# Optimization experiments

Measured on AMD Instinct MI355X. Metric: run time of the kernel, lower is better.

Reference implementation:

```python
import jax, jax.numpy as jnp
import numpy as np

N_HEAD = 16
D_MODEL = 1024
D_K = 64
D_V = 64
LN_EPS = 1e-6


def setup_inputs() -> dict:
    key = jax.random.key(0)
    ks = jax.random.split(key, 10)
    B, S = 2, 2048
    scale = 0.02
    return {
        "q": jax.random.normal(ks[0], (B, S, D_MODEL), jnp.float32),
        "k": jax.random.normal(ks[1], (B, S, D_MODEL), jnp.float32),
        "v": jax.random.normal(ks[2], (B, S, D_MODEL), jnp.float32),
        "Wq": jax.random.normal(ks[3], (D_MODEL, N_HEAD * D_K), jnp.float32) * scale,
        "Wk": jax.random.normal(ks[4], (D_MODEL, N_HEAD * D_K), jnp.float32) * scale,
        "Wv": jax.random.normal(ks[5], (D_MODEL, N_HEAD * D_V), jnp.float32) * scale,
        "Wfc": jax.random.normal(ks[6], (N_HEAD * D_V, D_MODEL), jnp.float32) * scale,
        "bfc": jnp.zeros((D_MODEL,), jnp.float32),
        "gamma": jnp.ones((D_MODEL,), jnp.float32),
        "beta": jnp.zeros((D_MODEL,), jnp.float32),
    }


def reference(q, k, v, Wq, Wk, Wv, Wfc, bfc, gamma, beta):
    B, S, _ = q.shape
    residual = q
    # QKV projections, split into heads: [B, S, H, Dh]
    qh = (q @ Wq).reshape(B, S, N_HEAD, D_K)
    kh = (k @ Wk).reshape(B, S, N_HEAD, D_K)
    vh = (v @ Wv).reshape(B, S, N_HEAD, D_V)
    # scaled dot-product attention (explicit score matrix, as in source)
    temperature = jnp.asarray(D_K, qh.dtype) ** 0.5
    attn = jnp.einsum("bqhd,bkhd->bhqk", qh, kh) / temperature
    attn = jax.nn.softmax(attn, axis=-1)
    out = jnp.einsum("bhqk,bkhd->bqhd", attn, vh).reshape(B, S, N_HEAD * D_V)
    # output projection (dropout is identity in eval mode)
    out = out @ Wfc + bfc
    # residual + layernorm (eps=1e-6)
    x = out + residual
    mu = jnp.mean(x, axis=-1, keepdims=True)
    var = jnp.mean(jnp.square(x - mu), axis=-1, keepdims=True)
    return (x - mu) / jnp.sqrt(var + LN_EPS) * gamma + beta
```

## Files before the change

kernel.cpp:

```cpp
#include <hip/hip_runtime.h>

typedef float f32x4 __attribute__((ext_vector_type(4)));
typedef short short8 __attribute__((ext_vector_type(8)));
typedef short short4v __attribute__((ext_vector_type(4)));
typedef unsigned short ushort_t;

#define D_MODEL 1024
#define N_HEAD 16
#define SEQ 2048
#define BATCH 2
#define M_TOK 4096
#define HD 1024
#define QSCALE_L2E 0.1803368801111f

__device__ __forceinline__ ushort_t f2bf(float f) {
    union { float f; unsigned int u; } x; x.f = f;
    unsigned int r = x.u + 0x7fffu + ((x.u >> 16) & 1u);
    return (ushort_t)(r >> 16);
}
__device__ __forceinline__ ushort_t f2bf_fast(float f) {
    union { float f; unsigned int u; } x; x.f = f;
    return (ushort_t)((x.u + 0x8000u) >> 16);
}

__device__ __forceinline__ void async_copy16(const ushort_t* gptr, ushort_t* lptr) {
    __builtin_amdgcn_global_load_lds(
        (const __attribute__((address_space(1))) unsigned int*)gptr,
        (__attribute__((address_space(3))) unsigned int*)lptr, 16, 0, 0);
}

__global__ __launch_bounds__(256) void transpose_cast4(const float* __restrict__ w0,
                                                       const float* __restrict__ w1,
                                                       const float* __restrict__ w2,
                                                       const float* __restrict__ w3,
                                                       ushort_t* __restrict__ o0,
                                                       ushort_t* __restrict__ o1,
                                                       ushort_t* __restrict__ o2,
                                                       ushort_t* __restrict__ o3) {
    const int R = D_MODEL, C = D_MODEL;
    int z = blockIdx.z;
    const float* in = (z == 0) ? w0 : (z == 1) ? w1 : (z == 2) ? w2 : w3;
    ushort_t* out = (z == 0) ? o0 : (z == 1) ? o1 : (z == 2) ? o2 : o3;
    __shared__ ushort_t t[32][33];
    int bc = blockIdx.x * 32, br = blockIdx.y * 32;
    for (int i = threadIdx.y; i < 32; i += 8)
        t[i][threadIdx.x] = f2bf(in[(size_t)(br + i) * C + bc + threadIdx.x]);
    __syncthreads();
    for (int i = threadIdx.y; i < 32; i += 8)
        out[(size_t)(bc + i) * R + br + threadIdx.x] = t[threadIdx.x][i];
}

__global__ __launch_bounds__(256) void cast_bf16_3(const float* __restrict__ q,
                                                   const float* __restrict__ k,
                                                   const float* __restrict__ v,
                                                   ushort_t* __restrict__ qo,
                                                   ushort_t* __restrict__ ko,
                                                   ushort_t* __restrict__ vo) {
    int z = blockIdx.z;
    const float* s = (z == 0) ? q : (z == 1) ? k : v;
    ushort_t* d = (z == 0) ? qo : (z == 1) ? ko : vo;
    size_t i = ((size_t)blockIdx.x * 256 + threadIdx.x) * 8;
    float4 a = *(const float4*)(s + i);
    float4 b = *(const float4*)(s + i + 4);
    ushort_t tmp[8] = {f2bf(a.x), f2bf(a.y), f2bf(a.z), f2bf(a.w),
                       f2bf(b.x), f2bf(b.y), f2bf(b.z), f2bf(b.w)};
    *(short8*)(d + i) = *(short8*)tmp;
}

__global__ __launch_bounds__(256) void gemm_qkv(const ushort_t* __restrict__ qb,
                                                const ushort_t* __restrict__ kb,
                                                const ushort_t* __restrict__ vb,
                                                const ushort_t* __restrict__ wq,
                                                const ushort_t* __restrict__ wk,
                                                const ushort_t* __restrict__ wv,
                                                ushort_t* __restrict__ Qo,
                                                ushort_t* __restrict__ Ko,
                                                ushort_t* __restrict__ VtO) {
    __shared__ ushort_t As[128 * 32];
    __shared__ ushort_t Bs[128 * 32];
    const int z = blockIdx.z;
    const ushort_t* A = (z == 0) ? qb : (z == 1) ? kb : vb;
    const ushort_t* Bt = (z == 0) ? wq : (z == 1) ? wk : wv;
    const int tid = threadIdx.x;
    const int wave = tid >> 6, lane = tid & 63;
    const int quad = lane >> 4, l16 = lane & 15;
    const int m0 = blockIdx.y * 128, n0 = blockIdx.x * 128;
    const int wm = (wave >> 1) * 64, wn = (wave & 1) * 64;
    const int K = D_MODEL, N = D_MODEL;

    f32x4 acc[4][4];
    for (int i = 0; i < 4; ++i)
        for (int j = 0; j < 4; ++j) acc[i][j] = (f32x4){0.f, 0.f, 0.f, 0.f};

    for (int kk = 0; kk < K; kk += 32) {
        __syncthreads();
        #pragma unroll
        for (int c = 0; c < 2; ++c) {
            int flat = ((wave * 2 + c) * 64 + lane) * 8;
            int r = flat >> 5, col = flat & 31;
            async_copy16(Bt + (size_t)(n0 + r) * K + kk + col, &Bs[(wave * 2 + c) * 512]);
            async_copy16(A + (size_t)(m0 + r) * K + kk + col, &As[(wave * 2 + c) * 512]);
        }
        __syncthreads();
        short8 af[4], bfr[4];
        #pragma unroll
        for (int i = 0; i < 4; ++i)
            af[i] = *(const short8*)&As[(wm + i * 16 + l16) * 32 + quad * 8];
        #pragma unroll
        for (int j = 0; j < 4; ++j)
            bfr[j] = *(const short8*)&Bs[(wn + j * 16 + l16) * 32 + quad * 8];
        #pragma unroll
        for (int i = 0; i < 4; ++i)
            #pragma unroll
            for (int j = 0; j < 4; ++j)
                acc[i][j] = __builtin_amdgcn_mfma_f32_16x16x32_bf16(af[i], bfr[j], acc[i][j], 0, 0, 0);
    }
    if (z == 2) {
        #pragma unroll
        for (int i = 0; i < 4; ++i)
            #pragma unroll
            for (int j = 0; j < 4; ++j) {
                int n = n0 + wn + j * 16 + l16;
                int m = m0 + wm + i * 16 + quad * 4;
                ushort_t tmp[4];
                #pragma unroll
                for (int r = 0; r < 4; ++r) tmp[r] = f2bf(acc[i][j][r]);
                *(short4v*)&VtO[(size_t)n * M_TOK + m] = *(short4v*)tmp;
            }
    } else {
        ushort_t* C = (z == 0) ? Qo : Ko;
        const float scale = (z == 0) ? QSCALE_L2E : 1.0f;
        #pragma unroll
        for (int i = 0; i < 4; ++i)
            #pragma unroll
            for (int j = 0; j < 4; ++j) {
                int n = n0 + wn + j * 16 + l16;
                #pragma unroll
                for (int r = 0; r < 4; ++r) {
                    int m = m0 + wm + i * 16 + quad * 4 + r;
                    C[(size_t)m * N + n] = f2bf(acc[i][j][r] * scale);
                }
            }
    }
}

__global__ __launch_bounds__(256) void gemm_fc(const ushort_t* __restrict__ A,
                                               const ushort_t* __restrict__ Bt,
                                               float* __restrict__ Cf,
                                               const float* __restrict__ bias,
                                               const float* __restrict__ resid) {
    __shared__ ushort_t As[128 * 32];
    __shared__ ushort_t Bs[128 * 32];
    const int tid = threadIdx.x;
    const int wave = tid >> 6, lane = tid & 63;
    const int quad = lane >> 4, l16 = lane & 15;
    const int m0 = blockIdx.y * 128, n0 = blockIdx.x * 128;
    const int wm = (wave >> 1) * 64, wn = (wave & 1) * 64;
    const int K = D_MODEL, N = D_MODEL;

    f32x4 acc[4][4];
    for (int i = 0; i < 4; ++i)
        for (int j = 0; j < 4; ++j) acc[i][j] = (f32x4){0.f, 0.f, 0.f, 0.f};

    for (int kk = 0; kk < K; kk += 32) {
        __syncthreads();
        #pragma unroll
        for (int c = 0; c < 2; ++c) {
            int flat = ((wave * 2 + c) * 64 + lane) * 8;
            int r = flat >> 5, col = flat & 31;
            async_copy16(Bt + (size_t)(n0 + r) * K + kk + col, &Bs[(wave * 2 + c) * 512]);
            async_copy16(A + (size_t)(m0 + r) * K + kk + col, &As[(wave * 2 + c) * 512]);
        }
        __syncthreads();
        short8 af[4], bfr[4];
        #pragma unroll
        for (int i = 0; i < 4; ++i)
            af[i] = *(const short8*)&As[(wm + i * 16 + l16) * 32 + quad * 8];
        #pragma unroll
        for (int j = 0; j < 4; ++j)
            bfr[j] = *(const short8*)&Bs[(wn + j * 16 + l16) * 32 + quad * 8];
        #pragma unroll
        for (int i = 0; i < 4; ++i)
            #pragma unroll
            for (int j = 0; j < 4; ++j)
                acc[i][j] = __builtin_amdgcn_mfma_f32_16x16x32_bf16(af[i], bfr[j], acc[i][j], 0, 0, 0);
    }
    #pragma unroll
    for (int i = 0; i < 4; ++i)
        #pragma unroll
        for (int j = 0; j < 4; ++j) {
            int n = n0 + wn + j * 16 + l16;
            #pragma unroll
            for (int r = 0; r < 4; ++r) {
                int m = m0 + wm + i * 16 + quad * 4 + r;
                Cf[(size_t)m * N + n] = acc[i][j][r] + bias[n] + resid[(size_t)m * N + n];
            }
        }
}

__global__ __launch_bounds__(256, 3) void attn64(const ushort_t* __restrict__ Qh,
                                                 const ushort_t* __restrict__ Kh,
                                                 const ushort_t* __restrict__ Vt,
                                                 ushort_t* __restrict__ O) {
    __shared__ ushort_t KVs[16768];
    __shared__ float lsb[4 * 64];
    const int tid = threadIdx.x;
    const int wave = tid >> 6, lane = tid & 63;
    const int quad = lane >> 4, l16 = lane & 15;
    const int b = blockIdx.z, h = blockIdx.y, qt = blockIdx.x;
    const size_t base = (size_t)b * SEQ * HD + h * 64;
    const ushort_t* Qb = Qh + base + (size_t)(qt * 64) * HD;
    const ushort_t* Kb = Kh + base;
    const ushort_t* Vb = Vt + (size_t)(h * 64) * M_TOK + (size_t)b * SEQ;

    ushort_t* Kw = KVs + wave * 2048;
    ushort_t* Vw = KVs + 8192 + wave * 2048;

    short8 qf[4][2];
    #pragma unroll
    for (int nt = 0; nt < 4; ++nt)
        #pragma unroll
        for (int s = 0; s < 2; ++s)
            qf[nt][s] = *(const short8*)(Qb + (size_t)(nt * 16 + l16) * HD + s * 32 + quad * 8);

    f32x4 oacc[4][4];
    #pragma unroll
    for (int nt = 0; nt < 4; ++nt)
        #pragma unroll
        for (int dt = 0; dt < 4; ++dt) oacc[nt][dt] = (f32x4){0.f, 0.f, 0.f, 0.f};
    float lsum[4] = {0.f, 0.f, 0.f, 0.f};

    const ushort_t* Kg = Kb + (size_t)(wave * 16 + (lane >> 2)) * HD + (lane & 3) * 8;
    const ushort_t* Vg = Vb + (size_t)(lane >> 1) * M_TOK + wave * 16 + (lane & 1) * 8;
    ushort_t* KL = Kw + lane * 8;
    ushort_t* VL = Vw + lane * 8;

    #pragma unroll
    for (int c = 0; c < 2; ++c) {
        async_copy16(Kg + c * 32, KL + c * 512);
        async_copy16(Vg + (size_t)c * 32 * M_TOK, VL + c * 512);
    }

    #pragma unroll 2
    for (int kt = 0; kt < SEQ / 64; ++kt) {
        const int buf = kt & 1;
        __builtin_amdgcn_s_waitcnt(0x0F70);
        if (kt < SEQ / 64 - 1) {
            #pragma unroll
            for (int c = 0; c < 2; ++c) {
                async_copy16(Kg + (size_t)(kt + 1) * 64 * HD + c * 32,
                             KL + (buf ^ 1) * 1024 + c * 512);
                async_copy16(Vg + (size_t)c * 32 * M_TOK + (kt + 1) * 64,
                             VL + (buf ^ 1) * 1024 + c * 512);
            }
        }
        short8 kf[2];
        #pragma unroll
        for (int s = 0; s < 2; ++s)
            kf[s] = *(const short8*)&Kw[buf * 1024 + s * 512 + l16 * 32 + quad * 8];
        short4v vf[4];
        #pragma unroll
        for (int dt = 0; dt < 4; ++dt)
            vf[dt] = *(const short4v*)&Vw[buf * 1024 + (dt * 16 + l16) * 16 + quad * 4];

        f32x4 sacc[4];
        #pragma unroll
        for (int nt = 0; nt < 4; ++nt) sacc[nt] = (f32x4){0.f, 0.f, 0.f, 0.f};
        #pragma unroll
        for (int s = 0; s < 2; ++s)
            #pragma unroll
            for (int nt = 0; nt < 4; ++nt)
                sacc[nt] = __builtin_amdgcn_mfma_f32_16x16x32_bf16(kf[s], qf[nt][s], sacc[nt], 0, 0, 0);

        short4v pf[4];
        #pragma unroll
        for (int nt = 0; nt < 4; ++nt) {
            ushort_t tmp[4];
            #pragma unroll
            for (int i = 0; i < 4; ++i) {
                float pv = exp2f(sacc[nt][i]);
                lsum[nt] += pv;
                tmp[i] = f2bf_fast(pv);
            }
            pf[nt] = *(short4v*)tmp;
        }
        #pragma unroll
        for (int nt = 0; nt < 4; ++nt)
            #pragma unroll
            for (int dt = 0; dt < 4; ++dt)
                oacc[nt][dt] = __builtin_amdgcn_mfma_f32_16x16x16bf16_1k(pf[nt], vf[dt], oacc[nt][dt], 0, 0, 0);
    }

    #pragma unroll
    for (int nt = 0; nt < 4; ++nt) {
        lsum[nt] += __shfl_xor(lsum[nt], 16, 64);
        lsum[nt] += __shfl_xor(lsum[nt], 32, 64);
    }
    if (quad == 0) {
        #pragma unroll
        for (int nt = 0; nt < 4; ++nt) lsb[wave * 64 + nt * 16 + l16] = lsum[nt];
    }
    __syncthreads();

    float* R0 = (float*)KVs;
    float* R1 = R0 + 64 * 65;
    {
        float* R = (wave & 1) ? R1 : R0;
        if (wave < 2) {
            #pragma unroll
            for (int nt = 0; nt < 4; ++nt)
                #pragma unroll
                for (int dt = 0; dt < 4; ++dt)
                    #pragma unroll
                    for (int i = 0; i < 4; ++i)
                        R[(nt * 16 + quad * 4 + i) * 65 + dt * 16 + l16] = oacc[nt][dt][i];
        }
        __syncthreads();
        if (wave >= 2) {
            #pragma unroll
            for (int nt = 0; nt < 4; ++nt)
                #pragma unroll
                for (int dt = 0; dt < 4; ++dt)
                    #pragma unroll
                    for (int i = 0; i < 4; ++i)
                        R[(nt * 16 + quad * 4 + i) * 65 + dt * 16 + l16] += oacc[nt][dt][i];
        }
        __syncthreads();
    }
    float inv[4];
    #pragma unroll
    for (int i = 0; i < 4; ++i) {
        int qrow = wave * 16 + quad * 4 + i;
        float t = lsb[qrow] + lsb[64 + qrow] + lsb[128 + qrow] + lsb[192 + qrow];
        inv[i] = 1.f / t;
    }
    ushort_t* Ob = O + base + (size_t)(qt * 64) * HD;
    #pragma unroll
    for (int i = 0; i < 4; ++i) {
        int qrow = wave * 16 + quad * 4 + i;
        #pragma unroll
        for (int dt = 0; dt < 4; ++dt) {
            int d = dt * 16 + l16;
            float val = R0[qrow * 65 + d] + R1[qrow * 65 + d];
            Ob[(size_t)qrow * HD + d] = f2bf(val * inv[i]);
        }
    }
}

__global__ __launch_bounds__(256) void ln_kernel(float* __restrict__ x,
                                                 const float* __restrict__ gamma,
                                                 const float* __restrict__ beta) {
    const int D = D_MODEL;
    float* xr = x + (size_t)blockIdx.x * D;
    const int tid = threadIdx.x;
    float4 v = *(const float4*)(xr + tid * 4);
    float s = v.x + v.y + v.z + v.w;
    float s2 = v.x * v.x + v.y * v.y + v.z * v.z + v.w * v.w;
    #pragma unroll
    for (int off = 1; off < 64; off <<= 1) {
        s += __shfl_xor(s, off, 64);
        s2 += __shfl_xor(s2, off, 64);
    }
    __shared__ float ws1[4], ws2[4];
    int wave = tid >> 6, lane = tid & 63;
    if (lane == 0) { ws1[wave] = s; ws2[wave] = s2; }
    __syncthreads();
    s = ws1[0] + ws1[1] + ws1[2] + ws1[3];
    s2 = ws2[0] + ws2[1] + ws2[2] + ws2[3];
    float mean = s * (1.f / D);
    float var = s2 * (1.f / D) - mean * mean;
    float rstd = rsqrtf(var + 1e-6f);
    float4 g = *(const float4*)(gamma + tid * 4);
    float4 bt = *(const float4*)(beta + tid * 4);
    float4 o;
    o.x = (v.x - mean) * rstd * g.x + bt.x;
    o.y = (v.y - mean) * rstd * g.y + bt.y;
    o.z = (v.z - mean) * rstd * g.z + bt.z;
    o.w = (v.w - mean) * rstd * g.w + bt.w;
    *(float4*)(xr + tid * 4) = o;
}

extern "C" void kernel_launch(void* const* d_in, const int* in_sizes, int n_in,
                              void* d_out, int out_size, void* d_ws, size_t ws_size,
                              hipStream_t stream) {
    const float* q = (const float*)d_in[0];
    const float* k = (const float*)d_in[1];
    const float* v = (const float*)d_in[2];
    const float* Wq = (const float*)d_in[3];
    const float* Wk = (const float*)d_in[4];
    const float* Wv = (const float*)d_in[5];
    const float* Wfc = (const float*)d_in[6];
    const float* bfc = (const float*)d_in[7];
    const float* gamma = (const float*)d_in[8];
    const float* beta = (const float*)d_in[9];
    float* out = (float*)d_out;

    char* ws = (char*)d_ws;
    const size_t MB = 1u << 20;
    ushort_t* WqT  = (ushort_t*)(ws + 0 * MB);
    ushort_t* WkT  = (ushort_t*)(ws + 2 * MB);
    ushort_t* WvT  = (ushort_t*)(ws + 4 * MB);
    ushort_t* WfcT = (ushort_t*)(ws + 6 * MB);
    ushort_t* qb   = (ushort_t*)(ws + 8 * MB);
    ushort_t* kb   = (ushort_t*)(ws + 16 * MB);
    ushort_t* vb   = (ushort_t*)(ws + 24 * MB);
    ushort_t* Qh   = (ushort_t*)(ws + 32 * MB);
    ushort_t* Kh   = (ushort_t*)(ws + 40 * MB);
    ushort_t* Vt   = (ushort_t*)(ws + 48 * MB);
    ushort_t* Oh   = (ushort_t*)(ws + 8 * MB);

    const int M = M_TOK, D = D_MODEL;
    transpose_cast4<<<dim3(D / 32, D / 32, 4), dim3(32, 8), 0, stream>>>(
        Wq, Wk, Wv, Wfc, WqT, WkT, WvT, WfcT);

    cast_bf16_3<<<dim3(M * D / (256 * 8), 1, 3), 256, 0, stream>>>(q, k, v, qb, kb, vb);

    gemm_qkv<<<dim3(D / 128, M / 128, 3), 256, 0, stream>>>(qb, kb, vb, WqT, WkT, WvT, Qh, Kh, Vt);

    attn64<<<dim3(SEQ / 64, N_HEAD, BATCH), 256, 0, stream>>>(Qh, Kh, Vt, Oh);

    gemm_fc<<<dim3(D / 128, M / 128), 256, 0, stream>>>(Oh, WfcT, out, bfc, q);

    ln_kernel<<<M, 256, 0, stream>>>(out, gamma, beta);
}
```

Before: 271.9 us.

## Load K to registers, triple-buffer swizzled V in attention, shrink FC tile

In the attention kernel, K fragments now go straight from global memory into registers with one-tile-ahead prefetch. V is triple-buffered in LDS and read with a rotated (swizzled) quad layout that matches a swizzled Vt write in the QKV GEMM epilogue, which is meant to reduce LDS bank conflicts. exp2f becomes the hardware builtin. Separately, the FC GEMM tile goes from 128x128 to 128x64, doubling the block count for better occupancy on many CUs.

Result: faster. 258.0 us (-5.1%).

```diff
diff --git a/kernel.cpp b/kernel.cpp
--- a/kernel.cpp
+++ b/kernel.cpp
@@ -11,6 +11,7 @@
 #define BATCH 2
 #define M_TOK 4096
 #define HD 1024
+#define NT 32
 #define QSCALE_L2E 0.1803368801111f
 
 __device__ __forceinline__ ushort_t f2bf(float f) {
@@ -121,11 +122,12 @@
             #pragma unroll
             for (int j = 0; j < 4; ++j) {
                 int n = n0 + wn + j * 16 + l16;
-                int m = m0 + wm + i * 16 + quad * 4;
+                int mBase = m0 + wm + i * 16;
+                int quadR = (quad + (n >> 2)) & 3;
                 ushort_t tmp[4];
                 #pragma unroll
                 for (int r = 0; r < 4; ++r) tmp[r] = f2bf(acc[i][j][r]);
-                *(short4v*)&VtO[(size_t)n * M_TOK + m] = *(short4v*)tmp;
+                *(short4v*)&VtO[(size_t)n * M_TOK + mBase + quadR * 4] = *(short4v*)tmp;
             }
     } else {
         ushort_t* C = (z == 0) ? Qo : Ko;
@@ -150,49 +152,53 @@
                                                const float* __restrict__ bias,
                                                const float* __restrict__ resid) {
     __shared__ ushort_t As[128 * 32];
-    __shared__ ushort_t Bs[128 * 32];
+    __shared__ ushort_t Bs[64 * 32];
     const int tid = threadIdx.x;
     const int wave = tid >> 6, lane = tid & 63;
     const int quad = lane >> 4, l16 = lane & 15;
-    const int m0 = blockIdx.y * 128, n0 = blockIdx.x * 128;
-    const int wm = (wave >> 1) * 64, wn = (wave & 1) * 64;
+    const int m0 = blockIdx.y * 128, n0 = blockIdx.x * 64;
     const int K = D_MODEL, N = D_MODEL;
 
-    f32x4 acc[4][4];
-    for (int i = 0; i < 4; ++i)
+    f32x4 acc[2][4];
+    for (int i = 0; i < 2; ++i)
         for (int j = 0; j < 4; ++j) acc[i][j] = (f32x4){0.f, 0.f, 0.f, 0.f};
 
     for (int kk = 0; kk < K; kk += 32) {
         __syncthreads();
         #pragma unroll
         for (int c = 0; c < 2; ++c) {
-            int flat = ((wave * 2 + c) * 64 + lane) * 8;
+            int g = wave * 2 + c;
+            int flat = (g * 64 + lane) * 8;
             int r = flat >> 5, col = flat & 31;
-            async_copy16(Bt + (size_t)(n0 + r) * K + kk + col, &Bs[(wave * 2 + c) * 512]);
-            async_copy16(A + (size_t)(m0 + r) * K + kk + col, &As[(wave * 2 + c) * 512]);
-        }
-        __syncthreads();
-        short8 af[4], bfr[4];
-        #pragma unroll
-        for (int i = 0; i < 4; ++i)
-            af[i] = *(const short8*)&As[(wm + i * 16 + l16) * 32 + quad * 8];
+            async_copy16(A + (size_t)(m0 + r) * K + kk + col, &As[g * 512]);
+        }
+        {
+            int flat = (wave * 64 + lane) * 8;
+            int r = flat >> 5, col = flat & 31;
+            async_copy16(Bt + (size_t)(n0 + r) * K + kk + col, &Bs[wave * 512]);
+        }
+        __syncthreads();
+        short8 af[2], bfr[4];
+        #pragma unroll
+        for (int i = 0; i < 2; ++i)
+            af[i] = *(const short8*)&As[(wave * 32 + i * 16 + l16) * 32 + quad * 8];
         #pragma unroll
         for (int j = 0; j < 4; ++j)
-            bfr[j] = *(const short8*)&Bs[(wn + j * 16 + l16) * 32 + quad * 8];
-        #pragma unroll
-        for (int i = 0; i < 4; ++i)
+            bfr[j] = *(const short8*)&Bs[(j * 16 + l16) * 32 + quad * 8];
+        #pragma unroll
+        for (int i = 0; i < 2; ++i)
             #pragma unroll
             for (int j = 0; j < 4; ++j)
                 acc[i][j] = __builtin_amdgcn_mfma_f32_16x16x32_bf16(af[i], bfr[j], acc[i][j], 0, 0, 0);
     }
     #pragma unroll
-    for (int i = 0; i < 4; ++i)
+    for (int i = 0; i < 2; ++i)
         #pragma unroll
         for (int j = 0; j < 4; ++j) {
-            int n = n0 + wn + j * 16 + l16;
+            int n = n0 + j * 16 + l16;
             #pragma unroll
             for (int r = 0; r < 4; ++r) {
-                int m = m0 + wm + i * 16 + quad * 4 + r;
+                int m = m0 + wave * 32 + i * 16 + quad * 4 + r;
                 Cf[(size_t)m * N + n] = acc[i][j][r] + bias[n] + resid[(size_t)m * N + n];
             }
         }
@@ -202,8 +208,7 @@
                                                  const ushort_t* __restrict__ Kh,
                                                  const ushort_t* __restrict__ Vt,
                                                  ushort_t* __restrict__ O) {
-    __shared__ ushort_t KVs[16768];
-    __shared__ float lsb[4 * 64];
+    __shared__ __align__(16) char smem[34304];
     const int tid = threadIdx.x;
     const int wave = tid >> 6, lane = tid & 63;
     const int quad = lane >> 4, l16 = lane & 15;
@@ -213,8 +218,8 @@
     const ushort_t* Kb = Kh + base;
     const ushort_t* Vb = Vt + (size_t)(h * 64) * M_TOK + (size_t)b * SEQ;
 
-    ushort_t* Kw = KVs + wave * 2048;
-    ushort_t* Vw = KVs + 8192 + wave * 2048;
+    ushort_t* Vw = (ushort_t*)smem + wave * 3072;
+    float* lsb = (float*)(smem + 33280);
 
     short8 qf[4][2];
     #pragma unroll
@@ -230,47 +235,51 @@
         for (int dt = 0; dt < 4; ++dt) oacc[nt][dt] = (f32x4){0.f, 0.f, 0.f, 0.f};
     float lsum[4] = {0.f, 0.f, 0.f, 0.f};
 
-    const ushort_t* Kg = Kb + (size_t)(wave * 16 + (lane >> 2)) * HD + (lane & 3) * 8;
+    const ushort_t* Kr = Kb + (size_t)(wave * 16 + l16) * HD + quad * 8;
     const ushort_t* Vg = Vb + (size_t)(lane >> 1) * M_TOK + wave * 16 + (lane & 1) * 8;
-    ushort_t* KL = Kw + lane * 8;
-    ushort_t* VL = Vw + lane * 8;
-
-    #pragma unroll
-    for (int c = 0; c < 2; ++c) {
-        async_copy16(Kg + c * 32, KL + c * 512);
-        async_copy16(Vg + (size_t)c * 32 * M_TOK, VL + c * 512);
-    }
-
-    #pragma unroll 2
-    for (int kt = 0; kt < SEQ / 64; ++kt) {
-        const int buf = kt & 1;
-        __builtin_amdgcn_s_waitcnt(0x0F70);
-        if (kt < SEQ / 64 - 1) {
-            #pragma unroll
-            for (int c = 0; c < 2; ++c) {
-                async_copy16(Kg + (size_t)(kt + 1) * 64 * HD + c * 32,
-                             KL + (buf ^ 1) * 1024 + c * 512);
-                async_copy16(Vg + (size_t)c * 32 * M_TOK + (kt + 1) * 64,
-                             VL + (buf ^ 1) * 1024 + c * 512);
-            }
-        }
-        short8 kf[2];
+    ushort_t* VLd = Vw + lane * 8;
+
+    short8 kf0[2], kf1[2];
+    #pragma unroll
+    for (int s = 0; s < 2; ++s) kf0[s] = *(const short8*)(Kr + s * 32);
+    #pragma unroll
+    for (int c = 0; c < 2; ++c)
+        async_copy16(Vg + (size_t)c * 32 * M_TOK, VLd + c * 512);
+    #pragma unroll
+    for (int c = 0; c < 2; ++c)
+        async_copy16(Vg + (size_t)c * 32 * M_TOK + 64, VLd + 1024 + c * 512);
+
+    ushort_t *vb0 = Vw, *vb1 = Vw + 1024, *vb2 = Vw + 2048;
+    const int rot = (l16 >> 2) & 3;
+
+    for (int kt = 0; kt < NT; ++kt) {
+        if (kt == NT - 1) __builtin_amdgcn_s_waitcnt(0x0F70);
+        else              __builtin_amdgcn_s_waitcnt(0x0F72);
+
+        if (kt + 1 < NT) {
+            #pragma unroll
+            for (int s = 0; s < 2; ++s)
+                kf1[s] = *(const short8*)(Kr + (size_t)(kt + 1) * 64 * HD + s * 32);
+        }
+        if (kt + 2 < NT) {
+            #pragma unroll
+            for (int c = 0; c < 2; ++c)
+                async_copy16(Vg + (size_t)c * 32 * M_TOK + (kt + 2) * 64, vb2 + lane * 8 + c * 512);
+        }
+
+        short4v vf[4];
+        #pragma unroll
+        for (int dt = 0; dt < 4; ++dt)
+            vf[dt] = *(const short4v*)&vb0[(dt * 16 + l16) * 16 + (((quad + rot) & 3) * 4)];
+
+        f32x4 sacc[4];
+        #pragma unroll
+        for (int nt = 0; nt < 4; ++nt) sacc[nt] = (f32x4){0.f, 0.f, 0.f, 0.f};
         #pragma unroll
         for (int s = 0; s < 2; ++s)
-            kf[s] = *(const short8*)&Kw[buf * 1024 + s * 512 + l16 * 32 + quad * 8];
-        short4v vf[4];
-        #pragma unroll
-        for (int dt = 0; dt < 4; ++dt)
-            vf[dt] = *(const short4v*)&Vw[buf * 1024 + (dt * 16 + l16) * 16 + quad * 4];
-
-        f32x4 sacc[4];
-        #pragma unroll
-        for (int nt = 0; nt < 4; ++nt) sacc[nt] = (f32x4){0.f, 0.f, 0.f, 0.f};
-        #pragma unroll
-        for (int s = 0; s < 2; ++s)
             #pragma unroll
             for (int nt = 0; nt < 4; ++nt)
-                sacc[nt] = __builtin_amdgcn_mfma_f32_16x16x32_bf16(kf[s], qf[nt][s], sacc[nt], 0, 0, 0);
+                sacc[nt] = __builtin_amdgcn_mfma_f32_16x16x32_bf16(kf0[s], qf[nt][s], sacc[nt], 0, 0, 0);
 
         short4v pf[4];
         #pragma unroll
@@ -278,7 +287,7 @@
             ushort_t tmp[4];
             #pragma unroll
             for (int i = 0; i < 4; ++i) {
-                float pv = exp2f(sacc[nt][i]);
+                float pv = __builtin_amdgcn_exp2f(sacc[nt][i]);
                 lsum[nt] += pv;
                 tmp[i] = f2bf_fast(pv);
             }
@@ -289,6 +298,9 @@
             #pragma unroll
             for (int dt = 0; dt < 4; ++dt)
                 oacc[nt][dt] = __builtin_amdgcn_mfma_f32_16x16x16bf16_1k(pf[nt], vf[dt], oacc[nt][dt], 0, 0, 0);
+
+        kf0[0] = kf1[0]; kf0[1] = kf1[1];
+        ushort_t* t = vb0; vb0 = vb1; vb1 = vb2; vb2 = t;
     }
 
     #pragma unroll
@@ -302,7 +314,7 @@
     }
     __syncthreads();
 
-    float* R0 = (float*)KVs;
+    float* R0 = (float*)smem;
     float* R1 = R0 + 64 * 65;
     {
         float* R = (wave & 1) ? R1 : R0;
@@ -419,7 +431,7 @@
 
     attn64<<<dim3(SEQ / 64, N_HEAD, BATCH), 256, 0, stream>>>(Qh, Kh, Vt, Oh);
 
-    gemm_fc<<<dim3(D / 128, M / 128), 256, 0, stream>>>(Oh, WfcT, out, bfc, q);
+    gemm_fc<<<dim3(D / 64, M / 128), 256, 0, stream>>>(Oh, WfcT, out, bfc, q);
 
     ln_kernel<<<M, 256, 0, stream>>>(out, gamma, beta);
 }
```
